# Performance work log

Hardware: AMD Instinct MI355X
Metric: run time of the kernel (lower is better)

Reference implementation:

```python
import jax, jax.numpy as jnp
import numpy as np

HIDDEN = 4096       # in_features of gate/up proj
INTER = 11008       # intermediate_size (per projection)
GROUP = 128         # GPTQ group size
B, S = 4, 2048
NIB = jnp.uint32(0xF)


def _pack_rows(nib):
    """Pack 4-bit values along rows: [8*R, C] uint32 -> [R, C] uint32."""
    r = nib.reshape(-1, 8, nib.shape[-1])
    shifts = (jnp.arange(8, dtype=jnp.uint32) * 4)[None, :, None]
    return jnp.sum(r << shifts, axis=1, dtype=jnp.uint32)  # disjoint bits -> sum == OR


def _pack_cols(nib):
    """Pack 4-bit values along cols: [G, 8*C] uint32 -> [G, C] uint32."""
    r = nib.reshape(nib.shape[0], -1, 8)
    shifts = (jnp.arange(8, dtype=jnp.uint32) * 4)[None, None, :]
    return jnp.sum(r << shifts, axis=2, dtype=jnp.uint32)


def setup_inputs() -> dict:
    key = jax.random.key(0)
    ks = jax.random.split(key, 7)
    n_groups = HIDDEN // GROUP          # 32 groups for gate_up
    n_groups_d = INTER // GROUP         # 86 groups for down

    x = jax.random.normal(ks[0], (B, S, HIDDEN), jnp.float32)

    # gate_up_proj: in=HIDDEN, out=2*INTER
    nib_w_gu = jax.random.randint(ks[1], (HIDDEN, 2 * INTER), 0, 16).astype(jnp.uint32)
    nib_z_gu = jax.random.randint(ks[2], (n_groups, 2 * INTER), 0, 15).astype(jnp.uint32)
    qweight_gu = _pack_rows(nib_w_gu)                          # [HIDDEN//8, 2*INTER]
    qzeros_gu = _pack_cols(nib_z_gu)                           # [n_groups, 2*INTER//8]
    scales_gu = jax.random.uniform(ks[3], (n_groups, 2 * INTER), jnp.float32, 0.005, 0.02)
    g_idx_gu = (jnp.arange(HIDDEN, dtype=jnp.int32) // GROUP)

    # down_proj: in=INTER, out=HIDDEN
    nib_w_d = jax.random.randint(ks[4], (INTER, HIDDEN), 0, 16).astype(jnp.uint32)
    nib_z_d = jax.random.randint(ks[5], (n_groups_d, HIDDEN), 0, 15).astype(jnp.uint32)
    qweight_down = _pack_rows(nib_w_d)                         # [INTER//8, HIDDEN]
    qzeros_down = _pack_cols(nib_z_d)                          # [n_groups_d, HIDDEN//8]
    scales_down = jax.random.uniform(ks[6], (n_groups_d, HIDDEN), jnp.float32, 0.005, 0.02)
    g_idx_down = (jnp.arange(INTER, dtype=jnp.int32) // GROUP)

    return {
        "x": x,
        "qweight_gu": qweight_gu, "qzeros_gu": qzeros_gu,
        "scales_gu": scales_gu, "g_idx_gu": g_idx_gu,
        "qweight_down": qweight_down, "qzeros_down": qzeros_down,
        "scales_down": scales_down, "g_idx_down": g_idx_down,
    }


def _dequant(qw, qz, sc, g_idx):
    """GPTQ v2 dequant: W[i,j] = sc[g[i],j] * (wq[i,j] - (zq[g[i],j] + 1))."""
    shifts = jnp.arange(8, dtype=jnp.uint32) * 4
    # unpack qweight along rows: [R, C] -> [8*R, C]
    wq = ((qw[:, None, :] >> shifts[None, :, None]) & NIB)
    wq = wq.reshape(-1, qw.shape[1]).astype(jnp.float32)
    # unpack qzeros along cols: [G, C//8] -> [G, C]; +1 per GPTQ v2 convention
    zq = ((qz[:, :, None] >> shifts[None, None, :]) & NIB)
    zq = zq.reshape(qz.shape[0], -1).astype(jnp.float32) + 1.0
    return sc[g_idx] * (wq - zq[g_idx])  # [in, out]


def reference(x, qweight_gu, qzeros_gu, scales_gu, g_idx_gu,
              qweight_down, qzeros_down, scales_down, g_idx_down):
    w_gu = _dequant(qweight_gu, qzeros_gu, scales_gu, g_idx_gu)          # [HIDDEN, 2*INTER]
    inter = jnp.einsum('bsh,hf->bsf', x, w_gu)                            # [B,S,2*INTER]
    gate, up = inter[..., :INTER], inter[..., INTER:]
    h = jax.nn.silu(gate) * up                                            # SwiGLU
    w_d = _dequant(qweight_down, qzeros_down, scales_down, g_idx_down)   # [INTER, HIDDEN]
    return jnp.einsum('bsf,fh->bsh', h, w_d)
```

## Files before the change

kernel.cpp:

```cpp
#include <hip/hip_runtime.h>
#include <stdint.h>

#define HIDDEN 4096
#define INTER  11008
#define NTOK   8192
#define WROW   22016

typedef __bf16 bf16;
typedef __bf16 bf16x8 __attribute__((ext_vector_type(8)));
typedef _Float16 f16;
typedef _Float16 f16x2 __attribute__((ext_vector_type(2)));
typedef _Float16 f16x8 __attribute__((ext_vector_type(8)));
typedef float  f32x4  __attribute__((ext_vector_type(4)));
typedef unsigned int u32x4 __attribute__((ext_vector_type(4)));

__device__ __forceinline__ void gload16(const void* g, void* l) {
  __builtin_amdgcn_global_load_lds(
      (const __attribute__((address_space(1))) void*)g,
      (__attribute__((address_space(3))) void*)l, 16, 0, 0);
}
__device__ __forceinline__ void gload4(const void* g, void* l) {
  __builtin_amdgcn_global_load_lds(
      (const __attribute__((address_space(1))) void*)g,
      (__attribute__((address_space(3))) void*)l, 4, 0, 0);
}

__global__ __launch_bounds__(256) void cvt_f16_kernel(const float* __restrict__ x,
                                                      f16* __restrict__ y) {
  const int i = (blockIdx.x * 256 + threadIdx.x) * 8;
  f32x4 a = *(const f32x4*)(x + i);
  f32x4 b = *(const f32x4*)(x + i + 4);
  f16x8 v;
#pragma unroll
  for (int j = 0; j < 4; ++j) { v[2 * j] = (f16)a[j]; v[2 * j + 1] = (f16)b[j]; }
  *(f16x8*)(y + i) = v;
}

__global__ __launch_bounds__(256) void spak_kernel(const uint32_t* __restrict__ qz,
                                                   const float* __restrict__ sc,
                                                   uint32_t* __restrict__ outp) {
  const int idx = blockIdx.x * 256 + threadIdx.x;
  const int gq = idx / WROW;
  const int n = idx - gq * WROW;
  const int grp = n >> 5, win = n & 31;
  const int jg = (win < 16) ? grp * 16 + win : INTER + grp * 16 + (win - 16);
  const float s = sc[(size_t)gq * WROW + jg];
  const uint32_t z = (qz[(size_t)gq * (WROW / 8) + (jg >> 3)] >> ((jg & 7) * 4)) & 15u;
  union { f16 h[2]; uint32_t u; } a, b;
  a.h[0] = (f16)s; a.h[1] = (f16)s;
  b.h[0] = (f16)(float)(1025u + z); b.h[1] = b.h[0];
  outp[(size_t)idx * 2 + 0] = a.u;
  outp[(size_t)idx * 2 + 1] = b.u;
}

__global__ __launch_bounds__(256) void repackB_kernel(const uint32_t* __restrict__ qw,
                                                      uint32_t* __restrict__ outp) {
  const size_t idx = (size_t)blockIdx.x * 256 + threadIdx.x;
  const int c = (int)(idx & 2047);
  const int kt = (int)((idx >> 11) & 63);
  const int nb = (int)(idx >> 17);
  const int j = c & 3;
  const int chunk = c >> 2;
  const int r = chunk >> 6;
  const int wc = (chunk >> 4) & 3;
  const int fr = chunk & 15;
  const int col = wc * 32 + fr + (j & 1) * 16 + (j >> 1) * 128;
  const int n = nb * 256 + col;
  const int grp = n >> 5, win = n & 31;
  const int jg = (win < 16) ? grp * 16 + win : INTER + grp * 16 + (win - 16);
  outp[idx] = qw[(size_t)(kt * 8 + r) * WROW + jg];
}

__global__ __launch_bounds__(256) void dequant_kernel(const uint32_t* __restrict__ qw,
                                                      const uint32_t* __restrict__ qz,
                                                      const float* __restrict__ sc,
                                                      bf16* __restrict__ out,
                                                      int J, int Kout) {
  __shared__ __align__(16) bf16 T[64 * 256];
  const int tid = threadIdx.x;
  const int tx = tid & 63, ty = tid >> 6;
  const int j0 = blockIdx.x * 64, r0 = blockIdx.y * 32;
  const int j = j0 + tx;
  const int J8 = J >> 3;
#pragma unroll
  for (int i = 0; i < 8; ++i) {
    const int r = r0 + ty * 8 + i;
    const int g = r >> 4;
    const uint32_t w = qw[(size_t)r * J + j];
    const float s = sc[(size_t)g * J + j];
    const uint32_t zb = (qz[(size_t)g * J8 + (j >> 3)] >> ((j & 7) * 4)) & 15u;
    const float zoff = (float)(zb + 1u);
    bf16x8 v;
#pragma unroll
    for (int e = 0; e < 8; ++e) {
      const float wv = (float)((w >> (e * 4)) & 15u);
      v[e] = (bf16)(s * (wv - zoff));
    }
    const int lb = (tx * 512 + (ty * 8 + i) * 16) ^ ((tx & 31) << 4);
    *(bf16x8*)((char*)T + lb) = v;
  }
  __syncthreads();
#pragma unroll
  for (int u = 0; u < 8; ++u) {
    const int unit = u * 256 + tid;
    const int jj = unit >> 5;
    const int ob = (unit & 31) * 16;
    const int lb = (jj * 512 + ob) ^ ((jj & 31) << 4);
    bf16x8 v = *(const bf16x8*)((const char*)T + lb);
    *(bf16x8*)(out + (size_t)(j0 + jj) * Kout + r0 * 8 + (ob >> 1)) = v;
  }
}

#define OFF_BP 65536
#define OFF_SPK 81920

#define BAR __builtin_amdgcn_s_barrier()
#define LGKM0                                              \
  do {                                                     \
    asm volatile("s_waitcnt lgkmcnt(0)" ::: "memory");     \
    __builtin_amdgcn_sched_barrier(0);                     \
  } while (0)
#define VM2 asm volatile("s_waitcnt vmcnt(2)" ::: "memory")
#define VM3 asm volatile("s_waitcnt vmcnt(3)" ::: "memory")

#define STG_A(buf, h, tt)                                                      \
  do {                                                                         \
    gload16(sA00 + ((size_t)((h) * 128) * (HIDDEN * 2)) + (size_t)(tt) * 128,  \
            lds + (buf) * 32768 + (h) * 16384 + w * 1024);                     \
    gload16(sA00 + ((size_t)((h) * 128 + 64) * (HIDDEN * 2)) + (size_t)(tt) * 128, \
            lds + (buf) * 32768 + (h) * 16384 + 8192 + w * 1024);              \
  } while (0)

#define STG_B(buf, tt)                                                         \
  gload16(repk_src + (size_t)(tt) * 2048 + tid * 4,                            \
          lds + OFF_BP + (buf) * 8192 + tid * 16)

#define STG_SPK(gt)                                                           \
  gload4(spakg + ((size_t)(gt) * WROW + n0) * 2 + tid,                        \
         lds + OFF_SPK + ((gt) & 3) * 2048 + w * 256)

__device__ __forceinline__ f16x8 unpack8s(uint32_t u, f16x2 s2, f16x2 k2) {
  const uint32_t MSK = 0x000F000Fu, M = 0x64006400u;
  uint32_t q0 = (u & MSK) | M;
  uint32_t q1 = ((u >> 4) & MSK) | M;
  uint32_t q2 = ((u >> 8) & MSK) | M;
  uint32_t q3 = ((u >> 12) & MSK) | M;
  f16x2 w0 = (__builtin_bit_cast(f16x2, q0) - k2) * s2;
  f16x2 w1 = (__builtin_bit_cast(f16x2, q1) - k2) * s2;
  f16x2 w2 = (__builtin_bit_cast(f16x2, q2) - k2) * s2;
  f16x2 w3 = (__builtin_bit_cast(f16x2, q3) - k2) * s2;
  f16x8 r;
  r[0] = w0[0]; r[1] = w0[1]; r[2] = w1[0]; r[3] = w1[1];
  r[4] = w2[0]; r[5] = w2[1]; r[6] = w3[0]; r[7] = w3[1];
  return r;
}

#define UNP_SL(BV, WORD, NH, NJ, KK, C)                                        \
  do {                                                                         \
    BV[NJ][KK] = unpack8s(WORD, s2r[NH][NJ], k2r[NH][NJ]);                     \
    _Pragma("unroll") for (int mi = 0; mi < 4; ++mi)                           \
      acc[mi][C] = __builtin_amdgcn_mfma_f32_16x16x32_f16(                     \
          av[mi][KK], BV[NJ][KK], acc[mi][C], 0, 0, 0);                        \
  } while (0)

__global__ __launch_bounds__(512, 2) void gemm1q(const f16* __restrict__ A,
                                                 const uint32_t* __restrict__ repk,
                                                 const uint32_t* __restrict__ spakg,
                                                 bf16* __restrict__ H) {
  extern __shared__ char lds[];
  const int tid = threadIdx.x;
  const int lane = tid & 63, w = tid >> 6;
  const int wr = w >> 2, wc = w & 3;
  const int fr = lane & 15, fg = lane >> 4;
  constexpr int NT = HIDDEN / 64;

  const int wg = blockIdx.x;
  const int nb = wg % (WROW / 256), mb = wg / (WROW / 256);
  const int m0 = mb << 8, n0 = nb << 8;

  const int rbase = tid >> 3;
  const int cbyte0 = (tid & 7) * 16;
  const int cL0 = cbyte0 ^ ((rbase & 7) << 4);
  const char* sA00 = (const char*)A + (size_t)(m0 + rbase) * (size_t)(HIDDEN * 2) + cL0;

  const uint32_t* repk_src = repk + (size_t)nb * 64 * 2048;

  const int swz = (fr & 7) << 4;
  const int ck[2] = {(fg * 16) ^ swz, (64 + fg * 16) ^ swz};
  const int aro = (wr * 64 + fr) * 128;
  auto lda = [&](int buf, int mh, int mi, int kk) -> f16x8 {
    return *(const f16x8*)(lds + buf * 32768 + mh * 16384 + aro + mi * 2048 + ck[kk]);
  };
  const int c1b = ((fg * 4 + wc) * 16 + fr) * 16;
  const int ncol[2][2] = {{wc * 32 + fr, wc * 32 + 16 + fr},
                          {wc * 32 + 128 + fr, wc * 32 + 144 + fr}};

  f32x4 acc[8][4];
#pragma unroll
  for (int i = 0; i < 8; ++i)
#pragma unroll
    for (int j = 0; j < 4; ++j) acc[i][j] = (f32x4)0.0f;
  f16x8 av[4][2], bv[2][2], bv2[2][2];
  f16x2 s2r[2][2], k2r[2][2];

  STG_SPK(0);
  STG_A(0, 0, 0);
  STG_B(0, 0);
  STG_A(0, 1, 0);
  VM2;
  BAR;

  for (int t = 0; t < NT; ++t) {
    const int cb = t & 1, nx = cb ^ 1, g = t >> 1;
    const int t1 = (t + 1 < NT) ? t + 1 : 0;

#pragma unroll
    for (int mi = 0; mi < 4; ++mi) { av[mi][0] = lda(cb, 0, mi, 0); av[mi][1] = lda(cb, 0, mi, 1); }
    u32x4 v1 = *(const u32x4*)(lds + OFF_BP + cb * 8192 + c1b);
    u32x4 v2 = *(const u32x4*)(lds + OFF_BP + cb * 8192 + c1b + 4096);
    if ((t & 1) == 0) {
      const char* sp = lds + OFF_SPK + (g & 3) * 2048;
#pragma unroll
      for (int nh = 0; nh < 2; ++nh)
#pragma unroll
        for (int nj = 0; nj < 2; ++nj) {
          s2r[nh][nj] = *(const f16x2*)(sp + ncol[nh][nj] * 8);
          k2r[nh][nj] = *(const f16x2*)(sp + ncol[nh][nj] * 8 + 4);
        }
    }
    STG_A(nx, 0, t1);
    STG_B(nx, t1);
    VM3;
    BAR; LGKM0;
    __builtin_amdgcn_s_setprio(1);
    UNP_SL(bv,  v1.x, 0, 0, 0, 0);
    UNP_SL(bv,  v2.x, 0, 0, 1, 0);
    UNP_SL(bv,  v1.y, 0, 1, 0, 1);
    UNP_SL(bv,  v2.y, 0, 1, 1, 1);
    UNP_SL(bv2, v1.z, 1, 0, 0, 2);
    UNP_SL(bv2, v2.z, 1, 0, 1, 2);
    UNP_SL(bv2, v1.w, 1, 1, 0, 3);
    UNP_SL(bv2, v2.w, 1, 1, 1, 3);
    __builtin_amdgcn_s_setprio(0);
    __builtin_amdgcn_sched_barrier(0);
    BAR;

#pragma unroll
    for (int mi = 0; mi < 4; ++mi) { av[mi][0] = lda(cb, 1, mi, 0); av[mi][1] = lda(cb, 1, mi, 1); }
    if (t & 1) {
      const int gt = (g + 1 < 32) ? g + 1 : 31;
      STG_SPK(gt);
    }
    STG_A(nx, 1, t1);
    BAR; LGKM0;
    __builtin_amdgcn_s_setprio(1);
#pragma unroll
    for (int kk = 0; kk < 2; ++kk)
#pragma unroll
      for (int nj = 0; nj < 2; ++nj) {
#pragma unroll
        for (int mi = 0; mi < 4; ++mi)
          acc[4 + mi][nj] = __builtin_amdgcn_mfma_f32_16x16x32_f16(
              av[mi][kk], bv[nj][kk], acc[4 + mi][nj], 0, 0, 0);
#pragma unroll
        for (int mi = 0; mi < 4; ++mi)
          acc[4 + mi][2 + nj] = __builtin_amdgcn_mfma_f32_16x16x32_f16(
              av[mi][kk], bv2[nj][kk], acc[4 + mi][2 + nj], 0, 0, 0);
      }
    __builtin_amdgcn_s_setprio(0);
    __builtin_amdgcn_sched_barrier(0);
    VM2;
    BAR;
  }
  asm volatile("s_waitcnt vmcnt(0)" ::: "memory");

#pragma unroll
  for (int mh = 0; mh < 2; ++mh)
#pragma unroll
    for (int mi = 0; mi < 4; ++mi)
#pragma unroll
      for (int nh = 0; nh < 2; ++nh) {
        const f32x4 gv4 = acc[mh * 4 + mi][nh * 2];
        const f32x4 uv4 = acc[mh * 4 + mi][nh * 2 + 1];
        const int col = (n0 >> 1) + wc * 16 + nh * 64 + fr;
#pragma unroll
        for (int rr = 0; rr < 4; ++rr) {
          const int row = m0 + wr * 64 + mh * 128 + mi * 16 + fg * 4 + rr;
          const float gv = gv4[rr], uv = uv4[rr];
          H[(size_t)row * INTER + col] = (bf16)(gv / (1.0f + __expf(-gv)) * uv);
        }
      }
}

#define OFF_A2 0
#define OFF_B2 32768

#define STG2(mat, buf, h, t)                                                   \
  do {                                                                         \
    gload16(s##mat[h][0] + (size_t)(t) * 128,                                  \
            lds + (buf) * 65536 + OFF_##mat + (h) * 16384 + w * 1024);         \
    gload16(s##mat[h][1] + (size_t)(t) * 128,                                  \
            lds + (buf) * 65536 + OFF_##mat + (h) * 16384 + 8192 + w * 1024);  \
  } while (0)
#define VM6 asm volatile("s_waitcnt vmcnt(6)" ::: "memory")

#define MFMA_Q2(MH, NH)                                                        \
  do {                                                                         \
    __builtin_amdgcn_s_setprio(1);                                             \
    _Pragma("unroll") for (int kk = 0; kk < 2; ++kk) {                         \
      _Pragma("unroll") for (int nj = 0; nj < 2; ++nj) {                       \
        _Pragma("unroll") for (int mi = 0; mi < 4; ++mi) {                     \
          acc[(MH)*4 + mi][(NH)*2 + nj] = __builtin_amdgcn_mfma_f32_16x16x32_bf16( \
              av[mi][kk], bv[nj][kk], acc[(MH)*4 + mi][(NH)*2 + nj], 0, 0, 0); \
        }                                                                      \
      }                                                                        \
    }                                                                          \
    __builtin_amdgcn_s_setprio(0);                                             \
    __builtin_amdgcn_sched_barrier(0);                                         \
  } while (0)

template <int K, int NT, int NNB>
__global__ __launch_bounds__(512, 2) void gemm8p(const bf16* __restrict__ A,
                                                 const bf16* __restrict__ Bm,
                                                 float* __restrict__ O) {
  extern __shared__ char lds[];
  const int tid = threadIdx.x;
  const int lane = tid & 63, w = tid >> 6;
  const int wr = w >> 2, wc = w & 3;
  const int fr = lane & 15, fg = lane >> 4;

  const int wg = blockIdx.x;
  const int nb = wg % NNB, mb = wg / NNB;
  const int m0 = mb << 8, n0 = nb << 8;

  const char* sA2[2][2];
  const char* sB2[2][2];
#pragma unroll
  for (int h = 0; h < 2; ++h)
#pragma unroll
    for (int l = 0; l < 2; ++l) {
      const int d = h * 16384 + (l * 512 + tid) * 16;
      const int r = d >> 7;
      const int cL = (d & 127) ^ ((r & 7) << 4);
      sA2[h][l] = (const char*)A + (size_t)(m0 + r) * (size_t)(K * 2) + cL;
      sB2[h][l] = (const char*)Bm + (size_t)(n0 + r) * (size_t)(K * 2) + cL;
    }

  const int swz = (fr & 7) << 4;
  const int ck[2] = {(fg * 16) ^ swz, (64 + fg * 16) ^ swz};
  const int aro = (wr * 64 + fr) * 128;
  const int bro = OFF_B2 + (wc * 32 + fr) * 128;

  auto lda = [&](int buf, int mh, int mi, int kk) -> bf16x8 {
    return *(const bf16x8*)(lds + buf * 65536 + mh * 16384 + aro + mi * 2048 + ck[kk]);
  };
  auto ldb = [&](int buf, int nh, int nj, int kk) -> bf16x8 {
    return *(const bf16x8*)(lds + buf * 65536 + bro + nh * 16384 + nj * 2048 + ck[kk]);
  };

  f32x4 acc[8][4];
#pragma unroll
  for (int i = 0; i < 8; ++i)
#pragma unroll
    for (int j = 0; j < 4; ++j) acc[i][j] = (f32x4)0.0f;
  bf16x8 av[4][2], bv[2][2];

  STG2(A2, 0, 0, 0);
  STG2(B2, 0, 0, 0);
  STG2(B2, 0, 1, 0);
  STG2(A2, 0, 1, 0);
  STG2(A2, 1, 0, 1);
  STG2(B2, 1, 1, 1);
  STG2(A2, 1, 1, 1);
  VM6;
  BAR;

  for (int t = 0; t < NT; ++t) {
    const int cb = t & 1, nx = cb ^ 1;
    const int t1 = (t + 1 < NT) ? t + 1 : 0;
    const int t2 = (t + 2 < NT) ? t + 2 : 0;

#pragma unroll
    for (int mi = 0; mi < 4; ++mi) { av[mi][0] = lda(cb, 0, mi, 0); av[mi][1] = lda(cb, 0, mi, 1); }
#pragma unroll
    for (int nj = 0; nj < 2; ++nj) { bv[nj][0] = ldb(cb, 0, nj, 0); bv[nj][1] = ldb(cb, 0, nj, 1); }
    STG2(B2, nx, 0, t1);
    BAR; LGKM0;
    MFMA_Q2(0, 0);
    BAR;

#pragma unroll
    for (int nj = 0; nj < 2; ++nj) { bv[nj][0] = ldb(cb, 1, nj, 0); bv[nj][1] = ldb(cb, 1, nj, 1); }
    STG2(A2, cb, 0, t2);
    BAR; LGKM0;
    MFMA_Q2(0, 1);
    BAR;

#pragma unroll
    for (int mi = 0; mi < 4; ++mi) { av[mi][0] = lda(cb, 1, mi, 0); av[mi][1] = lda(cb, 1, mi, 1); }
    STG2(B2, cb, 1, t2);
    BAR; LGKM0;
    MFMA_Q2(1, 1);
    BAR;

#pragma unroll
    for (int nj = 0; nj < 2; ++nj) { bv[nj][0] = ldb(cb, 0, nj, 0); bv[nj][1] = ldb(cb, 0, nj, 1); }
    STG2(A2, cb, 1, t2);
    VM6;
    BAR; LGKM0;
    MFMA_Q2(1, 0);
    BAR;
  }

#pragma unroll
  for (int mh = 0; mh < 2; ++mh)
#pragma unroll
    for (int mi = 0; mi < 4; ++mi)
#pragma unroll
      for (int nh = 0; nh < 2; ++nh)
#pragma unroll
        for (int nj = 0; nj < 2; ++nj) {
          const f32x4 a = acc[mh * 4 + mi][nh * 2 + nj];
          const int col = n0 + wc * 32 + nh * 128 + nj * 16 + fr;
#pragma unroll
          for (int rr = 0; rr < 4; ++rr) {
            const int row = m0 + wr * 64 + mh * 128 + mi * 16 + fg * 4 + rr;
            __builtin_nontemporal_store(a[rr], &O[(size_t)row * HIDDEN + col]);
          }
        }
}

extern "C" void kernel_launch(void* const* d_in, const int* in_sizes, int n_in,
                              void* d_out, int out_size, void* d_ws, size_t ws_size,
                              hipStream_t stream) {
  (void)in_sizes; (void)n_in; (void)out_size; (void)ws_size;
  const float*    x     = (const float*)d_in[0];
  const uint32_t* qw_gu = (const uint32_t*)d_in[1];
  const uint32_t* qz_gu = (const uint32_t*)d_in[2];
  const float*    sc_gu = (const float*)d_in[3];
  const uint32_t* qw_d  = (const uint32_t*)d_in[5];
  const uint32_t* qz_d  = (const uint32_t*)d_in[6];
  const float*    sc_d  = (const float*)d_in[7];
  float*          out   = (float*)d_out;

  char* ws = (char*)d_ws;
  const size_t XB  = (size_t)NTOK * HIDDEN * 2;
  const size_t W2B = (size_t)HIDDEN * INTER * 2;
  const size_t HB  = (size_t)NTOK * INTER * 2;
  const size_t SPB = (size_t)32 * WROW * 2 * 4;
  f16*      xb    = (f16*)ws;
  bf16*     wt    = (bf16*)(ws + XB);
  bf16*     hb    = (bf16*)(ws + XB + W2B);
  uint32_t* spakg = (uint32_t*)(ws + XB + W2B + HB);
  uint32_t* repk  = (uint32_t*)(ws + XB + W2B + HB + SPB);

  hipFuncSetAttribute((const void*)&gemm1q,
                      hipFuncAttributeMaxDynamicSharedMemorySize, 90112);
  hipFuncSetAttribute((const void*)&gemm8p<INTER, INTER / 64, HIDDEN / 256>,
                      hipFuncAttributeMaxDynamicSharedMemorySize, 131072);

  cvt_f16_kernel<<<NTOK * HIDDEN / 2048, 256, 0, stream>>>(x, xb);
  spak_kernel<<<32 * WROW / 256, 256, 0, stream>>>(qz_gu, sc_gu, spakg);
  repackB_kernel<<<((WROW / 256) * 64 * 2048) / 256, 256, 0, stream>>>(qw_gu, repk);

  gemm1q<<<(WROW / 256) * (NTOK / 256), 512, 90112, stream>>>(xb, repk, spakg, hb);

  dequant_kernel<<<dim3(HIDDEN / 64, (INTER / 8) / 32), 256, 0, stream>>>(
      qw_d, qz_d, sc_d, wt, HIDDEN, INTER);
  gemm8p<INTER, INTER / 64, HIDDEN / 256>
      <<<(HIDDEN / 256) * (NTOK / 256), 512, 131072, stream>>>(hb, wt, out);
}
```

Baseline: 2.085 ms.

## Give each gemm1q wave a full-M 256x32 tile so B is dequantized once

Changes the gemm1q warp decomposition from a 2x4 grid (each wave owning 128 rows by 64 cols) to eight waves each owning all 256 rows and 32 columns, and reorders the repacked B layout to match. Each wave now unpacks only 4 B words per k-step instead of 8, which removes the duplicate dequantization that waves sharing the same columns used to do. In exchange, each wave reads all A rows from LDS, doubling A LDS traffic, and the extra LDS waits and MFMA phases may reduce overlap. The accumulator footprint stays the same size.

```diff
diff --git a/kernel.cpp b/kernel.cpp
--- a/kernel.cpp
+++ b/kernel.cpp
@@ -60,15 +60,15 @@
   const int kt = (int)((idx >> 11) & 63);
   const int nb = (int)(idx >> 17);
   const int j = c & 3;
-  const int chunk = c >> 2;
-  const int r = chunk >> 6;
-  const int wc = (chunk >> 4) & 3;
-  const int fr = chunk & 15;
-  const int col = wc * 32 + fr + (j & 1) * 16 + (j >> 1) * 128;
+  const int L = c >> 2;
+  const int w = L >> 6, fg = (L >> 4) & 3, fr = L & 15;
+  const int kk = j >> 1, nj = j & 1;
+  const int row = kt * 8 + kk * 4 + fg;
+  const int col = w * 32 + nj * 16 + fr;
   const int n = nb * 256 + col;
   const int grp = n >> 5, win = n & 31;
   const int jg = (win < 16) ? grp * 16 + win : INTER + grp * 16 + (win - 16);
-  outp[idx] = qw[(size_t)(kt * 8 + r) * WROW + jg];
+  outp[idx] = qw[(size_t)row * WROW + jg];
 }
 
 __global__ __launch_bounds__(256) void dequant_kernel(const uint32_t* __restrict__ qw,
@@ -155,13 +155,17 @@
   return r;
 }
 
-#define UNP_SL(BV, WORD, NH, NJ, KK, C)                                        \
-  do {                                                                         \
-    BV[NJ][KK] = unpack8s(WORD, s2r[NH][NJ], k2r[NH][NJ]);                     \
-    _Pragma("unroll") for (int mi = 0; mi < 4; ++mi)                           \
-      acc[mi][C] = __builtin_amdgcn_mfma_f32_16x16x32_f16(                     \
-          av[mi][KK], BV[NJ][KK], acc[mi][C], 0, 0, 0);                        \
-  } while (0)
+#define MFMA4(R, NJ, KK)                                                       \
+  _Pragma("unroll") for (int mi = 0; mi < 4; ++mi)                             \
+      acc[(R) + mi][NJ] = __builtin_amdgcn_mfma_f32_16x16x32_f16(              \
+          av[mi][KK], bv[NJ][KK], acc[(R) + mi][NJ], 0, 0, 0)
+
+#define MFMA16(R)                                                              \
+  _Pragma("unroll") for (int kk = 0; kk < 2; ++kk)                             \
+    _Pragma("unroll") for (int nj = 0; nj < 2; ++nj)                           \
+      _Pragma("unroll") for (int mi = 0; mi < 4; ++mi)                         \
+          acc[(R) + mi][nj] = __builtin_amdgcn_mfma_f32_16x16x32_f16(          \
+              av[mi][kk], bv[nj][kk], acc[(R) + mi][nj], 0, 0, 0)
 
 __global__ __launch_bounds__(512, 2) void gemm1q(const f16* __restrict__ A,
                                                  const uint32_t* __restrict__ repk,
@@ -170,7 +174,6 @@
   extern __shared__ char lds[];
   const int tid = threadIdx.x;
   const int lane = tid & 63, w = tid >> 6;
-  const int wr = w >> 2, wc = w & 3;
   const int fr = lane & 15, fg = lane >> 4;
   constexpr int NT = HIDDEN / 64;
 
@@ -187,21 +190,19 @@
 
   const int swz = (fr & 7) << 4;
   const int ck[2] = {(fg * 16) ^ swz, (64 + fg * 16) ^ swz};
-  const int aro = (wr * 64 + fr) * 128;
-  auto lda = [&](int buf, int mh, int mi, int kk) -> f16x8 {
-    return *(const f16x8*)(lds + buf * 32768 + mh * 16384 + aro + mi * 2048 + ck[kk]);
+  const int aro = fr * 128;
+  auto lda = [&](int buf, int mi, int kk) -> f16x8 {
+    return *(const f16x8*)(lds + buf * 32768 + mi * 2048 + aro + ck[kk]);
   };
-  const int c1b = ((fg * 4 + wc) * 16 + fr) * 16;
-  const int ncol[2][2] = {{wc * 32 + fr, wc * 32 + 16 + fr},
-                          {wc * 32 + 128 + fr, wc * 32 + 144 + fr}};
-
-  f32x4 acc[8][4];
-#pragma unroll
-  for (int i = 0; i < 8; ++i)
-#pragma unroll
-    for (int j = 0; j < 4; ++j) acc[i][j] = (f32x4)0.0f;
-  f16x8 av[4][2], bv[2][2], bv2[2][2];
-  f16x2 s2r[2][2], k2r[2][2];
+  const int ncol2[2] = {w * 32 + fr, w * 32 + 16 + fr};
+
+  f32x4 acc[16][2];
+#pragma unroll
+  for (int i = 0; i < 16; ++i)
+#pragma unroll
+    for (int j = 0; j < 2; ++j) acc[i][j] = (f32x4)0.0f;
+  f16x8 av[4][2], bv[2][2];
+  f16x2 s2r[2], k2r[2];
 
   STG_SPK(0);
   STG_A(0, 0, 0);
@@ -215,38 +216,42 @@
     const int t1 = (t + 1 < NT) ? t + 1 : 0;
 
 #pragma unroll
-    for (int mi = 0; mi < 4; ++mi) { av[mi][0] = lda(cb, 0, mi, 0); av[mi][1] = lda(cb, 0, mi, 1); }
-    u32x4 v1 = *(const u32x4*)(lds + OFF_BP + cb * 8192 + c1b);
-    u32x4 v2 = *(const u32x4*)(lds + OFF_BP + cb * 8192 + c1b + 4096);
+    for (int mi = 0; mi < 4; ++mi) { av[mi][0] = lda(cb, mi, 0); av[mi][1] = lda(cb, mi, 1); }
+    u32x4 vv = *(const u32x4*)(lds + OFF_BP + cb * 8192 + tid * 16);
     if ((t & 1) == 0) {
       const char* sp = lds + OFF_SPK + (g & 3) * 2048;
 #pragma unroll
-      for (int nh = 0; nh < 2; ++nh)
-#pragma unroll
-        for (int nj = 0; nj < 2; ++nj) {
-          s2r[nh][nj] = *(const f16x2*)(sp + ncol[nh][nj] * 8);
-          k2r[nh][nj] = *(const f16x2*)(sp + ncol[nh][nj] * 8 + 4);
-        }
+      for (int nj = 0; nj < 2; ++nj) {
+        s2r[nj] = *(const f16x2*)(sp + ncol2[nj] * 8);
+        k2r[nj] = *(const f16x2*)(sp + ncol2[nj] * 8 + 4);
+      }
     }
     STG_A(nx, 0, t1);
     STG_B(nx, t1);
     VM3;
     BAR; LGKM0;
     __builtin_amdgcn_s_setprio(1);
-    UNP_SL(bv,  v1.x, 0, 0, 0, 0);
-    UNP_SL(bv,  v2.x, 0, 0, 1, 0);
-    UNP_SL(bv,  v1.y, 0, 1, 0, 1);
-    UNP_SL(bv,  v2.y, 0, 1, 1, 1);
-    UNP_SL(bv2, v1.z, 1, 0, 0, 2);
-    UNP_SL(bv2, v2.z, 1, 0, 1, 2);
-    UNP_SL(bv2, v1.w, 1, 1, 0, 3);
-    UNP_SL(bv2, v2.w, 1, 1, 1, 3);
+    bv[0][0] = unpack8s(vv.x, s2r[0], k2r[0]);
+    MFMA4(0, 0, 0);
+    bv[1][0] = unpack8s(vv.y, s2r[1], k2r[1]);
+    MFMA4(0, 1, 0);
+    bv[0][1] = unpack8s(vv.z, s2r[0], k2r[0]);
+    MFMA4(0, 0, 1);
+    bv[1][1] = unpack8s(vv.w, s2r[1], k2r[1]);
+    MFMA4(0, 1, 1);
     __builtin_amdgcn_s_setprio(0);
     __builtin_amdgcn_sched_barrier(0);
-    BAR;
-
-#pragma unroll
-    for (int mi = 0; mi < 4; ++mi) { av[mi][0] = lda(cb, 1, mi, 0); av[mi][1] = lda(cb, 1, mi, 1); }
+#pragma unroll
+    for (int mi = 0; mi < 4; ++mi) { av[mi][0] = lda(cb, 4 + mi, 0); av[mi][1] = lda(cb, 4 + mi, 1); }
+    LGKM0;
+    __builtin_amdgcn_s_setprio(1);
+    MFMA16(4);
+    __builtin_amdgcn_s_setprio(0);
+    __builtin_amdgcn_sched_barrier(0);
+    BAR;
+
+#pragma unroll
+    for (int mi = 0; mi < 4; ++mi) { av[mi][0] = lda(cb, 8 + mi, 0); av[mi][1] = lda(cb, 8 + mi, 1); }
     if (t & 1) {
       const int gt = (g + 1 < 32) ? g + 1 : 31;
       STG_SPK(gt);
@@ -254,19 +259,14 @@
     STG_A(nx, 1, t1);
     BAR; LGKM0;
     __builtin_amdgcn_s_setprio(1);
-#pragma unroll
-    for (int kk = 0; kk < 2; ++kk)
-#pragma unroll
-      for (int nj = 0; nj < 2; ++nj) {
-#pragma unroll
-        for (int mi = 0; mi < 4; ++mi)
-          acc[4 + mi][nj] = __builtin_amdgcn_mfma_f32_16x16x32_f16(
-              av[mi][kk], bv[nj][kk], acc[4 + mi][nj], 0, 0, 0);
-#pragma unroll
-        for (int mi = 0; mi < 4; ++mi)
-          acc[4 + mi][2 + nj] = __builtin_amdgcn_mfma_f32_16x16x32_f16(
-              av[mi][kk], bv2[nj][kk], acc[4 + mi][2 + nj], 0, 0, 0);
-      }
+    MFMA16(8);
+    __builtin_amdgcn_s_setprio(0);
+    __builtin_amdgcn_sched_barrier(0);
+#pragma unroll
+    for (int mi = 0; mi < 4; ++mi) { av[mi][0] = lda(cb, 12 + mi, 0); av[mi][1] = lda(cb, 12 + mi, 1); }
+    LGKM0;
+    __builtin_amdgcn_s_setprio(1);
+    MFMA16(12);
     __builtin_amdgcn_s_setprio(0);
     __builtin_amdgcn_sched_barrier(0);
     VM2;
@@ -274,22 +274,18 @@
   }
   asm volatile("s_waitcnt vmcnt(0)" ::: "memory");
 
-#pragma unroll
-  for (int mh = 0; mh < 2; ++mh)
-#pragma unroll
-    for (int mi = 0; mi < 4; ++mi)
-#pragma unroll
-      for (int nh = 0; nh < 2; ++nh) {
-        const f32x4 gv4 = acc[mh * 4 + mi][nh * 2];
-        const f32x4 uv4 = acc[mh * 4 + mi][nh * 2 + 1];
-        const int col = (n0 >> 1) + wc * 16 + nh * 64 + fr;
-#pragma unroll
-        for (int rr = 0; rr < 4; ++rr) {
-          const int row = m0 + wr * 64 + mh * 128 + mi * 16 + fg * 4 + rr;
-          const float gv = gv4[rr], uv = uv4[rr];
-          H[(size_t)row * INTER + col] = (bf16)(gv / (1.0f + __expf(-gv)) * uv);
-        }
-      }
+  const int col = (n0 >> 1) + w * 16 + fr;
+#pragma unroll
+  for (int mi = 0; mi < 16; ++mi) {
+    const f32x4 gv4 = acc[mi][0];
+    const f32x4 uv4 = acc[mi][1];
+#pragma unroll
+    for (int rr = 0; rr < 4; ++rr) {
+      const int row = m0 + mi * 16 + fg * 4 + rr;
+      const float gv = gv4[rr], uv = uv4[rr];
+      H[(size_t)row * INTER + col] = (bf16)(gv / (1.0f + __expf(-gv)) * uv);
+    }
+  }
 }
 
 #define OFF_A2 0
```

After: 2.034 ms. -2.4%, faster.
